# Kernel optimization log

Measured on AMD Instinct MI355X. Metric: run time of the kernel, lower is better.

The kernel has to match this reference:

```python
import jax, jax.numpy as jnp
import numpy as np

B, E, L = 8, 512, 8192
MAX_W = 4          # max_subword_block_width -> widths 1..3
KSIZE = 5          # conv_kernel_size
DS = 2             # downsample_rate


def setup_inputs() -> dict:
    key = jax.random.key(0)
    k0, k1, k2, k3 = jax.random.split(key, 4)
    x = jax.random.normal(k0, (B, E, L), dtype=jnp.float32)
    # Conv1d(E, E, KSIZE): weight [out_ch, in_ch, k], bias [out_ch]
    conv_w = jax.random.normal(k1, (E, E, KSIZE), dtype=jnp.float32) * (1.0 / np.sqrt(E * KSIZE))
    conv_b = jax.random.normal(k2, (E,), dtype=jnp.float32) * 0.01
    # Linear(E, 1, bias=False): stored as vector [E]
    score_w = jax.random.normal(k3, (E,), dtype=jnp.float32) * (1.0 / np.sqrt(E))
    return {"x": x, "conv_w": conv_w, "conv_b": conv_b, "score_w": score_w}


def reference(x, conv_w, conv_b, score_w):
    length = x.shape[-1]  # original length, captured BEFORE the valid conv (as in torch)
    # Pre-GBST conv, VALID padding -> length shrinks by KSIZE-1
    y = jax.lax.conv_general_dilated(
        x, conv_w, window_strides=(1,), padding="VALID",
        dimension_numbers=("NCH", "OIH", "NCH"))
    y = y + conv_b[None, :, None]

    seqs, scs = [], []
    for w in range(1, MAX_W):
        Lc = y.shape[-1]
        pad = (-Lc) % w
        yp = jnp.pad(y, ((0, 0), (0, 0), (0, pad))) if pad else y
        # avg_pool1d(kernel=w, stride=w) == reshape + mean (zero-pad counts in mean, matching torch)
        cand = yp.reshape(yp.shape[0], yp.shape[1], -1, w).mean(-1)  # [B,E,Nb]
        sc = jnp.einsum("ben,e->bn", cand, score_w)                  # [B,Nb]
        rs = jnp.repeat(cand, w, axis=-1)  # [B,E,Nb*w]
        rc = jnp.repeat(sc, w, axis=-1)    # [B,Nb*w]
        Lr = rs.shape[-1]
        if Lr < length:
            rs = jnp.pad(rs, ((0, 0), (0, 0), (0, length - Lr)))
            rc = jnp.pad(rc, ((0, 0), (0, length - Lr)))
        seqs.append(rs[:, :, :length])
        scs.append(rc[:, :length])
    seqs = jnp.stack(seqs, axis=-1)            # [B,E,L,W-1]
    scs = jnp.stack(scs, axis=-1)[:, None]     # [B,1,L,W-1]
    att = jax.nn.softmax(scs, axis=-1)
    out = (seqs * att).sum(-1)                 # [B,E,L]
    # Downsample via avg_pool1d(kernel=DS, stride=DS)
    b, e, l = out.shape
    out = out[:, :, :(l // DS) * DS].reshape(b, e, l // DS, DS).mean(-1)
    return out
```

## Files before the change

kernel.cpp:

```cpp
#include <hip/hip_runtime.h>
#include <math.h>

#define B_    8
#define E_    512
#define L_    8192
#define K_    5
#define LC    8188
#define LOUT  4096
#define LPAD  8256

typedef float  f32x4   __attribute__((ext_vector_type(4)));
typedef float  f32x16  __attribute__((ext_vector_type(16)));
typedef short  s16x4   __attribute__((ext_vector_type(4)));
typedef short  s16x8   __attribute__((ext_vector_type(8)));

__device__ __forceinline__ unsigned short f2bf(float f) {
    union { float f; unsigned u; } v; v.f = f;
    unsigned r = v.u + 0x7FFFu + ((v.u >> 16) & 1u);
    return (unsigned short)(r >> 16);
}
__device__ __forceinline__ float bf2f(unsigned short h) {
    union { unsigned u; float f; } v; v.u = ((unsigned)h) << 16;
    return v.f;
}

__global__ __launch_bounds__(256) void wt_kernel(const float* __restrict__ w,
                                                 unsigned short* __restrict__ Wtb) {
    int idx = blockIdx.x * 256 + threadIdx.x;
    if (idx >= E_ * E_ * K_) return;
    int i    = idx & (E_ - 1);
    int rest = idx >> 9;
    int e    = rest & (E_ - 1);
    int k    = rest >> 9;
    Wtb[idx] = f2bf(w[((size_t)e * E_ + i) * K_ + k]);
}

__global__ __launch_bounds__(256) void xt_kernel(const float* __restrict__ x,
                                                 unsigned short* __restrict__ xT) {
    __shared__ float s[64][65];
    const int b  = blockIdx.z;
    const int i0 = blockIdx.y * 64;
    const int t0 = blockIdx.x * 64;
    #pragma unroll
    for (int j = 0; j < 16; ++j) {
        int idx = threadIdx.x + j * 256;
        int r = idx >> 6, c = idx & 63;
        int t = t0 + c;
        s[c][r] = (t < L_) ? x[((size_t)b * E_ + i0 + r) * L_ + t] : 0.f;
    }
    __syncthreads();
    #pragma unroll
    for (int j = 0; j < 4; ++j) {
        int idx = threadIdx.x + j * 256;
        int tt = idx >> 4, ig = (idx & 15) * 4;
        s16x4 v;
        v[0] = (short)f2bf(s[tt][ig + 0]);
        v[1] = (short)f2bf(s[tt][ig + 1]);
        v[2] = (short)f2bf(s[tt][ig + 2]);
        v[3] = (short)f2bf(s[tt][ig + 3]);
        *(s16x4*)&xT[((size_t)b * LPAD + t0 + tt) * E_ + i0 + ig] = v;
    }
}

__global__ __launch_bounds__(256) void zero_z(float* __restrict__ z) {
    int idx = blockIdx.x * 256 + threadIdx.x;
    if (idx < (B_ * LC) / 4) ((f32x4*)z)[idx] = (f32x4)0.f;
}

__global__ __launch_bounds__(256, 2) void conv_mfma(const unsigned short* __restrict__ xT,
                                                    const unsigned short* __restrict__ Wtb,
                                                    const float* __restrict__ bias,
                                                    const float* __restrict__ sw,
                                                    unsigned short* __restrict__ y,
                                                    float* __restrict__ z) {
    __shared__ unsigned short Xs[520][40];
    __shared__ unsigned short Ws[K_][64][40];
    __shared__ float swb[128];

    const int tid  = threadIdx.x;
    const int nt   = blockIdx.x;
    const int b    = nt >> 4;
    const int tb   = (nt & 15) * 512;
    const int e0   = blockIdx.y * 64;
    const int wave = tid >> 6;
    const int lane = tid & 63;
    const int l32  = lane & 31;
    const int hi   = lane >> 5;
    const int wt0  = wave * 128;

    if (tid < 64)       swb[tid] = sw[e0 + tid];
    else if (tid < 128) swb[tid] = bias[e0 + tid - 64];

    f32x16 acc[2][4];
    #pragma unroll
    for (int es = 0; es < 2; ++es)
        #pragma unroll
        for (int ts = 0; ts < 4; ++ts) acc[es][ts] = (f32x16)0.f;

    const unsigned short* xbase = xT + ((size_t)b * LPAD + tb) * E_;

    s16x8 xpf[9];
    s16x8 wpf[5];

    auto load_tile = [&](int i0) {
        #pragma unroll
        for (int j = 0; j < 8; ++j) {
            int idx = tid + j * 256;
            int r = idx >> 2, c = idx & 3;
            xpf[j] = *(const s16x8*)(xbase + (size_t)r * E_ + i0 + c * 8);
        }
        {
            int idx = tid + 2048;
            if (idx < 2080) {
                int r = idx >> 2, c = idx & 3;
                xpf[8] = *(const s16x8*)(xbase + (size_t)r * E_ + i0 + c * 8);
            }
        }
        #pragma unroll
        for (int j = 0; j < 5; ++j) {
            int idx = tid + j * 256;
            int rl = idx >> 2, c = idx & 3;
            int k = rl >> 6, ep = rl & 63;
            wpf[j] = *(const s16x8*)(Wtb + ((size_t)(k * E_ + e0 + ep) * E_ + i0 + c * 8));
        }
    };
    auto store_tile = [&]() {
        #pragma unroll
        for (int j = 0; j < 8; ++j) {
            int idx = tid + j * 256;
            int r = idx >> 2, c = idx & 3;
            *(s16x8*)&Xs[r][c * 8] = xpf[j];
        }
        {
            int idx = tid + 2048;
            if (idx < 2080) {
                int r = idx >> 2, c = idx & 3;
                *(s16x8*)&Xs[r][c * 8] = xpf[8];
            }
        }
        #pragma unroll
        for (int j = 0; j < 5; ++j) {
            int idx = tid + j * 256;
            int rl = idx >> 2, c = idx & 3;
            int k = rl >> 6, ep = rl & 63;
            *(s16x8*)&Ws[k][ep][c * 8] = wpf[j];
        }
    };

    load_tile(0);
    for (int i0 = 0; i0 < E_; i0 += 32) {
        __syncthreads();
        store_tile();
        __syncthreads();
        if (i0 + 32 < E_) load_tile(i0 + 32);

        #pragma unroll
        for (int k = 0; k < K_; ++k) {
            #pragma unroll
            for (int kk = 0; kk < 2; ++kk) {
                const int co = kk * 16 + hi * 8;
                s16x8 a0 = *(const s16x8*)&Ws[k][l32][co];
                s16x8 a1 = *(const s16x8*)&Ws[k][32 + l32][co];
                #pragma unroll
                for (int ts = 0; ts < 4; ++ts) {
                    s16x8 bv = *(const s16x8*)&Xs[wt0 + ts * 32 + l32 + k][co];
                    acc[0][ts] = __builtin_amdgcn_mfma_f32_32x32x16_bf16(a0, bv, acc[0][ts], 0, 0, 0);
                    acc[1][ts] = __builtin_amdgcn_mfma_f32_32x32x16_bf16(a1, bv, acc[1][ts], 0, 0, 0);
                }
            }
        }
    }

    #pragma unroll
    for (int ts = 0; ts < 4; ++ts) {
        const int t = tb + wt0 + ts * 32 + l32;
        const bool tv = (t < LC);
        float zp = 0.f;
        #pragma unroll
        for (int es = 0; es < 2; ++es) {
            #pragma unroll
            for (int reg = 0; reg < 16; ++reg) {
                int er = es * 32 + (reg & 3) + 8 * (reg >> 2) + 4 * hi;
                float v = acc[es][ts][reg] + swb[64 + er];
                if (tv) y[((size_t)b * E_ + e0 + er) * LC + t] = f2bf(v);
                zp += swb[er] * v;
            }
        }
        zp += __shfl_xor(zp, 32);
        if (hi == 0 && tv) atomicAdd(&z[(size_t)b * LC + t], zp);
    }
}

#define DTILE 256
#define STAGE 520
__global__ __launch_bounds__(256) void out_kernel(const unsigned short* __restrict__ y,
                                                  const float* __restrict__ z,
                                                  float* __restrict__ out) {
    __shared__ float ys[STAGE];
    __shared__ float zs[STAGE];
    const int be = blockIdx.x;
    const int b  = be >> 9;
    const int d0 = blockIdx.y * DTILE;
    const int tb = d0 * 2;
    const unsigned short* yrow = y + (size_t)be * LC;
    const float* zrow = z + (size_t)b * LC;
    for (int i = threadIdx.x; i < STAGE; i += 256) {
        int t = tb - 2 + i;
        bool v = (t >= 0) && (t < LC);
        ys[i] = v ? bf2f(yrow[t]) : 0.f;
        zs[i] = v ? zrow[t] : 0.f;
    }
    __syncthreads();
    const int d = d0 + threadIdx.x;
    float o = 0.f;
    #pragma unroll
    for (int half = 0; half < 2; ++half) {
        int t = 2 * d + half;
        int j = t - tb + 2;
        float C1 = ys[j], S1 = zs[j];
        int i2 = (t & ~1) - tb + 2;
        float C2 = 0.5f * (ys[i2] + ys[i2 + 1]);
        float S2 = 0.5f * (zs[i2] + zs[i2 + 1]);
        int i3 = (t / 3) * 3 - tb + 2;
        float C3 = (ys[i3] + ys[i3 + 1] + ys[i3 + 2]) * (1.f / 3.f);
        float S3 = (zs[i3] + zs[i3 + 1] + zs[i3 + 2]) * (1.f / 3.f);
        float m  = fmaxf(S1, fmaxf(S2, S3));
        float a1 = __expf(S1 - m), a2 = __expf(S2 - m), a3 = __expf(S3 - m);
        o += (a1 * C1 + a2 * C2 + a3 * C3) / (a1 + a2 + a3);
    }
    out[(size_t)be * LOUT + d] = 0.5f * o;
}

extern "C" void kernel_launch(void* const* d_in, const int* in_sizes, int n_in,
                              void* d_out, int out_size, void* d_ws, size_t ws_size,
                              hipStream_t stream) {
    const float* x       = (const float*)d_in[0];
    const float* conv_w  = (const float*)d_in[1];
    const float* conv_b  = (const float*)d_in[2];
    const float* score_w = (const float*)d_in[3];
    float* out = (float*)d_out;

    unsigned short* base = (unsigned short*)d_ws;
    unsigned short* Wtb = base;
    unsigned short* xT  = Wtb + (size_t)K_ * E_ * E_;
    unsigned short* y   = xT + (size_t)B_ * LPAD * E_;
    float*          z   = (float*)(y + (size_t)B_ * E_ * LC);

    wt_kernel<<<dim3((E_ * E_ * K_ + 255) / 256), 256, 0, stream>>>(conv_w, Wtb);
    xt_kernel<<<dim3(LPAD / 64, E_ / 64, B_), 256, 0, stream>>>(x, xT);
    zero_z<<<dim3((B_ * LC / 4 + 255) / 256), 256, 0, stream>>>(z);
    conv_mfma<<<dim3(B_ * 16, E_ / 64), 256, 0, stream>>>(xT, Wtb, conv_b, score_w, y, z);
    out_kernel<<<dim3(B_ * E_, LOUT / DTILE), 256, 0, stream>>>(y, z, out);
}
```

Baseline: 448.6 us.

## Replace atomic score reduction with per-block partials and restage output kernel per row

The conv kernel now writes per-channel-block partial scores to separate buffers instead of atomically adding into a zeroed array, which removes the zeroing kernel and atomic contention. The output kernel processes a whole (batch, channel) row per block, staging y and the summed partial scores in shared memory. The transpose kernel uses vectorized float4 loads. The tradeoff is that every row block re-reads and sums eight partial score rows, which multiplies score traffic, and the larger shared footprint limits occupancy.

```diff
diff --git a/kernel.cpp b/kernel.cpp
--- a/kernel.cpp
+++ b/kernel.cpp
@@ -42,29 +42,28 @@
     const int i0 = blockIdx.y * 64;
     const int t0 = blockIdx.x * 64;
     #pragma unroll
-    for (int j = 0; j < 16; ++j) {
+    for (int j = 0; j < 4; ++j) {
         int idx = threadIdx.x + j * 256;
-        int r = idx >> 6, c = idx & 63;
-        int t = t0 + c;
-        s[c][r] = (t < L_) ? x[((size_t)b * E_ + i0 + r) * L_ + t] : 0.f;
+        int r  = idx >> 4;
+        int c4 = (idx & 15) * 4;
+        f32x4 v = (f32x4)0.f;
+        if (t0 < L_)
+            v = *(const f32x4*)&x[((size_t)b * E_ + i0 + r) * L_ + t0 + c4];
+        s[c4 + 0][r] = v[0]; s[c4 + 1][r] = v[1];
+        s[c4 + 2][r] = v[2]; s[c4 + 3][r] = v[3];
     }
     __syncthreads();
     #pragma unroll
     for (int j = 0; j < 4; ++j) {
         int idx = threadIdx.x + j * 256;
         int tt = idx >> 4, ig = (idx & 15) * 4;
-        s16x4 v;
-        v[0] = (short)f2bf(s[tt][ig + 0]);
-        v[1] = (short)f2bf(s[tt][ig + 1]);
-        v[2] = (short)f2bf(s[tt][ig + 2]);
-        v[3] = (short)f2bf(s[tt][ig + 3]);
-        *(s16x4*)&xT[((size_t)b * LPAD + t0 + tt) * E_ + i0 + ig] = v;
-    }
-}
-
-__global__ __launch_bounds__(256) void zero_z(float* __restrict__ z) {
-    int idx = blockIdx.x * 256 + threadIdx.x;
-    if (idx < (B_ * LC) / 4) ((f32x4*)z)[idx] = (f32x4)0.f;
+        s16x4 o;
+        o[0] = (short)f2bf(s[tt][ig + 0]);
+        o[1] = (short)f2bf(s[tt][ig + 1]);
+        o[2] = (short)f2bf(s[tt][ig + 2]);
+        o[3] = (short)f2bf(s[tt][ig + 3]);
+        *(s16x4*)&xT[((size_t)b * LPAD + t0 + tt) * E_ + i0 + ig] = o;
+    }
 }
 
 __global__ __launch_bounds__(256, 2) void conv_mfma(const unsigned short* __restrict__ xT,
@@ -72,7 +71,7 @@
                                                     const float* __restrict__ bias,
                                                     const float* __restrict__ sw,
                                                     unsigned short* __restrict__ y,
-                                                    float* __restrict__ z) {
+                                                    float* __restrict__ zpart) {
     __shared__ unsigned short Xs[520][40];
     __shared__ unsigned short Ws[K_][64][40];
     __shared__ float swb[128];
@@ -171,6 +170,7 @@
         }
     }
 
+    float* zrow = zpart + (((size_t)blockIdx.y * B_ + b) << 13);
     #pragma unroll
     for (int ts = 0; ts < 4; ++ts) {
         const int t = tb + wt0 + ts * 32 + l32;
@@ -187,48 +187,56 @@
             }
         }
         zp += __shfl_xor(zp, 32);
-        if (hi == 0 && tv) atomicAdd(&z[(size_t)b * LC + t], zp);
-    }
-}
-
-#define DTILE 256
-#define STAGE 520
+        if (hi == 0) zrow[t] = zp;
+    }
+}
+
+#define SYS 8200
 __global__ __launch_bounds__(256) void out_kernel(const unsigned short* __restrict__ y,
-                                                  const float* __restrict__ z,
+                                                  const float* __restrict__ zpart,
                                                   float* __restrict__ out) {
-    __shared__ float ys[STAGE];
-    __shared__ float zs[STAGE];
-    const int be = blockIdx.x;
-    const int b  = be >> 9;
-    const int d0 = blockIdx.y * DTILE;
-    const int tb = d0 * 2;
+    __shared__ float zs[SYS];
+    __shared__ unsigned short ys[SYS];
+    const int be  = blockIdx.x;
+    const int b   = be >> 9;
+    const int tid = threadIdx.x;
+
+    for (int i = LC + tid; i < SYS; i += 256) { zs[i] = 0.f; ys[i] = 0; }
     const unsigned short* yrow = y + (size_t)be * LC;
-    const float* zrow = z + (size_t)b * LC;
-    for (int i = threadIdx.x; i < STAGE; i += 256) {
-        int t = tb - 2 + i;
-        bool v = (t >= 0) && (t < LC);
-        ys[i] = v ? bf2f(yrow[t]) : 0.f;
-        zs[i] = v ? zrow[t] : 0.f;
+    for (int c = tid; c < 2047; c += 256)
+        *(s16x4*)&ys[c * 4] = *(const s16x4*)(yrow + c * 4);
+    const float* zb = zpart + ((size_t)b << 13);
+    for (int c = tid; c < 2047; c += 256) {
+        f32x4 s = (f32x4)0.f;
+        #pragma unroll
+        for (int p = 0; p < 8; ++p)
+            s += *(const f32x4*)(zb + ((size_t)(p * B_) << 13) + c * 4);
+        *(f32x4*)&zs[c * 4] = s;
     }
     __syncthreads();
-    const int d = d0 + threadIdx.x;
-    float o = 0.f;
-    #pragma unroll
-    for (int half = 0; half < 2; ++half) {
-        int t = 2 * d + half;
-        int j = t - tb + 2;
-        float C1 = ys[j], S1 = zs[j];
-        int i2 = (t & ~1) - tb + 2;
-        float C2 = 0.5f * (ys[i2] + ys[i2 + 1]);
-        float S2 = 0.5f * (zs[i2] + zs[i2 + 1]);
-        int i3 = (t / 3) * 3 - tb + 2;
-        float C3 = (ys[i3] + ys[i3 + 1] + ys[i3 + 2]) * (1.f / 3.f);
-        float S3 = (zs[i3] + zs[i3 + 1] + zs[i3 + 2]) * (1.f / 3.f);
-        float m  = fmaxf(S1, fmaxf(S2, S3));
-        float a1 = __expf(S1 - m), a2 = __expf(S2 - m), a3 = __expf(S3 - m);
-        o += (a1 * C1 + a2 * C2 + a3 * C3) / (a1 + a2 + a3);
-    }
-    out[(size_t)be * LOUT + d] = 0.5f * o;
+
+    float* orow = out + (size_t)be * LOUT;
+    #pragma unroll
+    for (int j = 0; j < 16; ++j) {
+        const int d = j * 256 + tid;
+        float o = 0.f;
+        #pragma unroll
+        for (int half = 0; half < 2; ++half) {
+            int t = 2 * d + half;
+            float C1 = bf2f(ys[t]);
+            float S1 = zs[t];
+            int i2 = t & ~1;
+            float C2 = 0.5f * (bf2f(ys[i2]) + bf2f(ys[i2 + 1]));
+            float S2 = 0.5f * (zs[i2] + zs[i2 + 1]);
+            int i3 = (t / 3) * 3;
+            float C3 = (bf2f(ys[i3]) + bf2f(ys[i3 + 1]) + bf2f(ys[i3 + 2])) * (1.f / 3.f);
+            float S3 = (zs[i3] + zs[i3 + 1] + zs[i3 + 2]) * (1.f / 3.f);
+            float m  = fmaxf(S1, fmaxf(S2, S3));
+            float a1 = __expf(S1 - m), a2 = __expf(S2 - m), a3 = __expf(S3 - m);
+            o += (a1 * C1 + a2 * C2 + a3 * C3) / (a1 + a2 + a3);
+        }
+        orow[d] = 0.5f * o;
+    }
 }
 
 extern "C" void kernel_launch(void* const* d_in, const int* in_sizes, int n_in,
@@ -244,11 +252,10 @@
     unsigned short* Wtb = base;
     unsigned short* xT  = Wtb + (size_t)K_ * E_ * E_;
     unsigned short* y   = xT + (size_t)B_ * LPAD * E_;
-    float*          z   = (float*)(y + (size_t)B_ * E_ * LC);
+    float*          zpart = (float*)(y + (size_t)B_ * E_ * LC);
 
     wt_kernel<<<dim3((E_ * E_ * K_ + 255) / 256), 256, 0, stream>>>(conv_w, Wtb);
     xt_kernel<<<dim3(LPAD / 64, E_ / 64, B_), 256, 0, stream>>>(x, xT);
-    zero_z<<<dim3((B_ * LC / 4 + 255) / 256), 256, 0, stream>>>(z);
-    conv_mfma<<<dim3(B_ * 16, E_ / 64), 256, 0, stream>>>(xT, Wtb, conv_b, score_w, y, z);
-    out_kernel<<<dim3(B_ * E_, LOUT / DTILE), 256, 0, stream>>>(y, z, out);
-}
+    conv_mfma<<<dim3(B_ * 16, E_ / 64), 256, 0, stream>>>(xT, Wtb, conv_b, score_w, y, zpart);
+    out_kernel<<<dim3(B_ * E_), 256, 0, stream>>>(y, zpart, out);
+}
```

Result: no change. 456.4 us (+1.7%).
